# Kernel optimization log

Measured on AMD Instinct MI355X. Metric: run time of the kernel, lower is better.

The kernel has to match this reference:

```python
import jax, jax.numpy as jnp
import numpy as np

CONT_FIELD = 13
CATE_FIELD = 26
VOCAB = 100000
EMB_DIM = 64
HIDDEN = [1024, 1024]
B = 16384
N_FIELDS = CONT_FIELD + CATE_FIELD            # 39
COMB = N_FIELDS * (N_FIELDS - 1) // 2         # 741
FIRST = EMB_DIM * N_FIELDS + COMB             # 3237

# upper-triangular pair indices (i < j), matching the module's rows/cols
_ROWS, _COLS = np.triu_indices(N_FIELDS, k=1)
ROWS = jnp.asarray(_ROWS)
COLS = jnp.asarray(_COLS)


def setup_inputs() -> dict:
    key = jax.random.key(0)
    ks = jax.random.split(key, 12)
    a = np.square(3.0 / (CATE_FIELD * EMB_DIM))
    inp = {
        "conts": jax.random.uniform(ks[0], (B, CONT_FIELD), dtype=jnp.float32),
        "cates": jax.random.randint(ks[1], (B, CATE_FIELD), 0, VOCAB),
        "combs": jax.random.normal(ks[2], (B, COMB), dtype=jnp.float32),
        "emb_table": jax.random.uniform(ks[3], (VOCAB, EMB_DIM), minval=-a, maxval=a, dtype=jnp.float32),
        "W1": jax.random.normal(ks[4], (FIRST, HIDDEN[0]), dtype=jnp.float32) * (6.0 / (FIRST + HIDDEN[0])) ** 0.5,
        "b1": jnp.zeros((HIDDEN[0],), jnp.float32),
        "ln1_g": jnp.ones((HIDDEN[0],), jnp.float32),
        "ln1_b": jnp.zeros((HIDDEN[0],), jnp.float32),
        "W2": jax.random.normal(ks[5], (HIDDEN[0], HIDDEN[1]), dtype=jnp.float32) * (6.0 / (HIDDEN[0] + HIDDEN[1])) ** 0.5,
        "b2": jnp.zeros((HIDDEN[1],), jnp.float32),
        "ln2_g": jnp.ones((HIDDEN[1],), jnp.float32),
        "ln2_b": jnp.zeros((HIDDEN[1],), jnp.float32),
        "Wout": jax.random.normal(ks[6], (HIDDEN[1], 1), dtype=jnp.float32) * (6.0 / (HIDDEN[1] + 1)) ** 0.5,
        "bout": jnp.zeros((1,), jnp.float32),
    }
    return inp


def _layernorm(x, g, b, eps=1e-5):
    mu = jnp.mean(x, axis=-1, keepdims=True)
    var = jnp.mean((x - mu) ** 2, axis=-1, keepdims=True)
    return (x - mu) * jax.lax.rsqrt(var + eps) * g + b


def reference(conts, cates, combs, emb_table, W1, b1, ln1_g, ln1_b,
              W2, b2, ln2_g, ln2_b, Wout, bout):
    # continuous-field embeddings: rows 0..CONT_FIELD-1 of the table, scaled by values
    cont_emb = emb_table[:CONT_FIELD][None, :, :] * conts[:, :, None]   # [B, 13, D]
    cate_emb = emb_table[cates]                                          # [B, 26, D]
    cc = jnp.concatenate([cont_emb, cate_emb], axis=1)                   # [B, 39, D]
    # pairwise inner products: full Gram then upper-triangle extraction
    gram = jnp.einsum("bfd,bgd->bfg", cc, cc)                            # [B, 39, 39]
    pairs = gram[:, ROWS, COLS]                                          # [B, 741]
    X = jnp.concatenate([cont_emb.reshape(cc.shape[0], -1),
                         cate_emb.reshape(cc.shape[0], -1),
                         pairs], axis=1)                                  # [B, 3237]
    X = jax.nn.relu(_layernorm(X @ W1 + b1, ln1_g, ln1_b))
    X = jax.nn.relu(_layernorm(X @ W2 + b2, ln2_g, ln2_b))
    logit = jax.nn.sigmoid(X @ Wout + bout)                               # [B, 1]
    return logit
```

## Files before the change

### kernel.cpp

```cpp
#include <hip/hip_runtime.h>
#include <hip/hip_bf16.h>

#define BATCH 16384
#define NH 1024
#define NF 39
#define CCLD 72
#define KX 2432
#define NPAIR 741
#define FEAT_BLOCKS (BATCH / 4)
#define WPREP_BX (KX / 32 + NH / 32)
#define WPREP_BLOCKS (WPREP_BX * (NH / 32))

typedef __attribute__((ext_vector_type(8))) short bf16x8;
typedef __attribute__((ext_vector_type(4))) float f32x4;

typedef const __attribute__((address_space(1))) unsigned int* gptr_t;
typedef __attribute__((address_space(3))) unsigned int* lptr_t;

__device__ __forceinline__ float bf2f(unsigned short u) {
  union { unsigned int i; float f; } c; c.i = ((unsigned int)u) << 16; return c.f;
}
__device__ __forceinline__ unsigned short f2bf(float f) {
  union { float f; unsigned int i; } c; c.f = f;
  unsigned int r = c.i + 0x7FFFu + ((c.i >> 16) & 1u);
  return (unsigned short)(r >> 16);
}

__global__ __launch_bounds__(256) void prep_kernel(
    const float* __restrict__ conts, const int* __restrict__ cates,
    const float* __restrict__ emb, unsigned short* __restrict__ X,
    const float* __restrict__ W1, const float* __restrict__ W2,
    unsigned short* __restrict__ W1t, unsigned short* __restrict__ W2t) {
  __shared__ __align__(16) unsigned char smem[33664];

  if (blockIdx.x >= FEAT_BLOCKS) {
    int wq = blockIdx.x - FEAT_BLOCKS;
    int bx = wq % WPREP_BX;
    int nb = (wq / WPREP_BX) * 32;
    float (*tile)[33] = (float(*)[33])smem;
    int tx = threadIdx.x & 31, ty = threadIdx.x >> 5;
    if (bx < KX / 32) {
      int kb = bx * 32;
#pragma unroll
      for (int i = 0; i < 32; i += 8) {
        int k = kb + ty + i;
        float v = 0.f;
        if (k < 13) {
          float s = 0.f;
#pragma unroll 8
          for (int d = 0; d < 64; ++d)
            s += emb[k * 64 + d] * W1[(size_t)(k * 64 + d) * NH + nb + tx];
          v = s;
        } else if (k >= 16 && k < 1680) {
          v = W1[(size_t)(832 + k - 16) * NH + nb + tx];
        } else if (k >= 1680 && k < 1680 + NPAIR) {
          v = W1[(size_t)(2496 + k - 1680) * NH + nb + tx];
        }
        tile[ty + i][tx] = v;
      }
      __syncthreads();
#pragma unroll
      for (int i = 0; i < 32; i += 8)
        W1t[(size_t)(nb + ty + i) * KX + kb + tx] = f2bf(tile[tx][ty + i]);
    } else {
      int kb = (bx - KX / 32) * 32;
#pragma unroll
      for (int i = 0; i < 32; i += 8)
        tile[ty + i][tx] = W2[(size_t)(kb + ty + i) * NH + nb + tx];
      __syncthreads();
#pragma unroll
      for (int i = 0; i < 32; i += 8)
        W2t[(size_t)(nb + ty + i) * NH + kb + tx] = f2bf(tile[tx][ty + i]);
    }
    return;
  }

  int wid = threadIdx.x >> 6, lane = threadIdx.x & 63;
  int b = (blockIdx.x << 2) | wid;
  unsigned short* my = (unsigned short*)smem + wid * (48 * CCLD);
  unsigned short* pw = (unsigned short*)(smem + 27648) + wid * 752;
  unsigned short* Xrow = X + (size_t)b * KX;

  int2 c2[13];
#pragma unroll
  for (int i = 0; i < 13; ++i)
    c2[i] = ((const int2*)(cates + b * 26))[i];
  float cf[13];
#pragma unroll
  for (int f = 0; f < 13; ++f) cf[f] = conts[b * 13 + f];
  float cemb[13];
#pragma unroll
  for (int f = 0; f < 13; ++f) cemb[f] = emb[f * 64 + lane];
  float g[26];
#pragma unroll
  for (int j = 0; j < 26; ++j) {
    int idx = (j & 1) ? c2[j >> 1].y : c2[j >> 1].x;
    g[j] = emb[(size_t)idx * 64 + lane];
  }
#pragma unroll
  for (int f = 0; f < 13; ++f)
    my[f * CCLD + lane] = f2bf(cemb[f] * cf[f]);
#pragma unroll
  for (int j = 0; j < 26; ++j)
    my[(13 + j) * CCLD + lane] = f2bf(g[j]);
#pragma unroll
  for (int f = NF; f < 48; ++f) my[f * CCLD + lane] = 0;
  if (lane < 16) Xrow[lane] = (lane < 13) ? f2bf(cf[lane]) : 0;
  if (lane < 752 - NPAIR) pw[NPAIR + lane] = 0;
  __syncthreads();

#pragma unroll
  for (int i = 0; i < 4; ++i) {
    int q = i * 64 + lane;
    if (q < 208)
      *(bf16x8*)&Xrow[16 + q * 8] =
          *(const bf16x8*)&my[(13 + (q >> 3)) * CCLD + (q & 7) * 8];
  }

  int r15 = lane & 15, hi = lane >> 4;
  bf16x8 fr[2][3];
#pragma unroll
  for (int t = 0; t < 3; ++t)
#pragma unroll
    for (int h = 0; h < 2; ++h)
      fr[h][t] = *(const bf16x8*)&my[(t * 16 + r15) * CCLD + h * 32 + hi * 8];

  f32x4 acc[3][3];
#pragma unroll
  for (int it = 0; it < 3; ++it)
#pragma unroll
    for (int jt = 0; jt < 3; ++jt)
      acc[it][jt] = (f32x4){0.f, 0.f, 0.f, 0.f};
#pragma unroll
  for (int h = 0; h < 2; ++h)
#pragma unroll
    for (int it = 0; it < 3; ++it)
#pragma unroll
      for (int jt = 0; jt < 3; ++jt)
        acc[it][jt] = __builtin_amdgcn_mfma_f32_16x16x32_bf16(
            fr[h][it], fr[h][jt], acc[it][jt], 0, 0, 0);

#pragma unroll
  for (int it = 0; it < 3; ++it)
#pragma unroll
    for (int jt = 0; jt < 3; ++jt) {
      int g_ = jt * 16 + r15;
#pragma unroll
      for (int r = 0; r < 4; ++r) {
        int f = it * 16 + hi * 4 + r;
        if (f < g_ && g_ < NF) {
          int p = f * 38 - ((f * (f - 1)) >> 1) + g_ - f - 1;
          pw[p] = f2bf(acc[it][jt][r]);
        }
      }
    }
  __syncthreads();

#pragma unroll
  for (int i = 0; i < 2; ++i) {
    int q = i * 64 + lane;
    if (q < 94)
      *(bf16x8*)&Xrow[1680 + q * 8] = *(const bf16x8*)&pw[q * 8];
  }
}

#define GLL(s_, d_) __builtin_amdgcn_global_load_lds((gptr_t)(s_), (lptr_t)(d_), 16, 0, 0)
#define RD(p_) (*(const bf16x8*)(p_))
#define DSTA(buf, h) (lds + (buf) * 32768 + (h) * 8192 + sd)
#define DSTB(buf, h) (lds + (buf) * 32768 + 16384 + (h) * 8192 + sd)
#define STG(dst, srcb, tau) do { \
    const unsigned short* _s = (srcb) + (size_t)(tau) * 64; \
    GLL(_s, dst); GLL(_s + (size_t)64 * K, (dst) + 4096); } while (0)
#define PHASE_BAR() do { \
    __builtin_amdgcn_s_barrier(); \
    asm volatile("s_waitcnt lgkmcnt(0)" ::: "memory"); \
    __builtin_amdgcn_sched_barrier(0); \
    __builtin_amdgcn_s_setprio(1); } while (0)
#define PHASE_END() do { \
    __builtin_amdgcn_s_setprio(0); \
    __builtin_amdgcn_s_barrier(); \
    __builtin_amdgcn_sched_barrier(0); } while (0)
#define MQ(I0, J0, AB, BB) do { \
    _Pragma("unroll") \
    for (int i_ = 0; i_ < 4; ++i_) \
      _Pragma("unroll") \
      for (int j_ = 0; j_ < 2; ++j_) { \
        acc[(I0) + i_][(J0) + j_] = __builtin_amdgcn_mfma_f32_16x16x32_bf16( \
            AB[i_][0], BB[j_][0], acc[(I0) + i_][(J0) + j_], 0, 0, 0); \
        acc[(I0) + i_][(J0) + j_] = __builtin_amdgcn_mfma_f32_16x16x32_bf16( \
            AB[i_][1], BB[j_][1], acc[(I0) + i_][(J0) + j_], 0, 0, 0); \
      } } while (0)

__global__ __launch_bounds__(512, 2) void gemm_8ph(
    const unsigned short* __restrict__ A, const unsigned short* __restrict__ Bt,
    const float* __restrict__ bias, unsigned short* __restrict__ Hout,
    int K, int NT) {
  __shared__ unsigned short lds[65536];

  int bid = blockIdx.x;
  int swz = (bid & 7) * 32 + (bid >> 3);
  int mb = swz >> 2, nb = swz & 3;
  size_t m0 = (size_t)mb * 256, n0 = (size_t)nb * 256;

  int tid = threadIdx.x, lane = tid & 63, w = tid >> 6;
  int wr = w >> 2, wc = w & 3;
  int r15 = lane & 15, hi = lane >> 4;

  int sr = tid >> 3;
  int ce = ((tid & 7) ^ (sr & 7)) << 3;
  int sd = tid * 8;
  const unsigned short* A0p = A + (m0 + sr) * (size_t)K + ce;
  const unsigned short* A1p = A0p + (size_t)128 * K;
  const unsigned short* B0p = Bt + (n0 + sr) * (size_t)K + ce;
  const unsigned short* B1p = B0p + (size_t)128 * K;

  int cbs = (((hi << 4) ^ ((r15 & 7) << 4)) >> 1);
  int rb0 = r15 * 64 + cbs;
  int rb1 = rb0 ^ 32;
  const unsigned short* aH = lds + wr * 8192;
  const unsigned short* bH = lds + 16384 + (wc >> 1) * 8192 + (wc & 1) * 4096;

  f32x4 acc[8][4];
#pragma unroll
  for (int m = 0; m < 8; ++m)
#pragma unroll
    for (int n = 0; n < 4; ++n) acc[m][n] = (f32x4){0.f, 0.f, 0.f, 0.f};

  bf16x8 a0[4][2], a1[4][2], bS[2][2], bR[2][2];

  {
    int t1 = (NT > 1) ? 1 : 0;
    STG(DSTB(0, 0), B0p, 0);
    STG(DSTB(0, 1), B1p, 0);
    STG(DSTA(0, 0), A0p, 0);
    STG(DSTA(0, 1), A1p, 0);
    STG(DSTB(1, 0), B0p, t1);
    STG(DSTB(1, 1), B1p, t1);
    asm volatile("s_waitcnt vmcnt(4)" ::: "memory");
    __builtin_amdgcn_s_barrier();
    __builtin_amdgcn_sched_barrier(0);
#pragma unroll
    for (int i = 0; i < 4; ++i) {
      a0[i][0] = RD(aH + i * 1024 + rb0);
      a0[i][1] = RD(aH + i * 1024 + rb1);
    }
  }

  for (int t = 0; t < NT; ++t) {
    int cur = t & 1, nxt = cur ^ 1;
    int ta = (t + 1 < NT) ? t + 1 : NT - 1;
    int tb = (t + 2 < NT) ? t + 2 : NT - 1;
    const unsigned short* aBn = aH + nxt * 32768;
    const unsigned short* bB = bH + cur * 32768;

#pragma unroll
    for (int j = 0; j < 2; ++j) {
      bS[j][0] = RD(bB + j * 1024 + rb0);
      bS[j][1] = RD(bB + j * 1024 + rb1);
    }
    STG(DSTA(nxt, 0), A0p, ta);
    PHASE_BAR();
    MQ(0, 0, a0, bS);
    PHASE_END();

#pragma unroll
    for (int j = 0; j < 2; ++j) {
      bR[j][0] = RD(bB + (2 + j) * 1024 + rb0);
      bR[j][1] = RD(bB + (2 + j) * 1024 + rb1);
    }
#pragma unroll
    for (int i = 0; i < 4; ++i) {
      a1[i][0] = RD(aH + cur * 32768 + (4 + i) * 1024 + rb0);
      a1[i][1] = RD(aH + cur * 32768 + (4 + i) * 1024 + rb1);
    }
    STG(DSTA(nxt, 1), A1p, ta);
    __builtin_amdgcn_s_barrier();
    asm volatile("s_waitcnt lgkmcnt(8)" ::: "memory");
    __builtin_amdgcn_sched_barrier(0);
    __builtin_amdgcn_s_setprio(1);
    MQ(0, 2, a0, bR);
    PHASE_END();

    STG(DSTB(cur, 0), B0p, tb);
    PHASE_BAR();
    MQ(4, 2, a1, bR);
    PHASE_END();

    STG(DSTB(cur, 1), B1p, tb);
    asm volatile("s_waitcnt vmcnt(4)" ::: "memory");
    __builtin_amdgcn_s_barrier();
#pragma unroll
    for (int i = 0; i < 4; ++i) {
      a0[i][0] = RD(aBn + i * 1024 + rb0);
      a0[i][1] = RD(aBn + i * 1024 + rb1);
    }
    __builtin_amdgcn_sched_barrier(0);
    __builtin_amdgcn_s_setprio(1);
    MQ(4, 0, a1, bS);
    PHASE_END();
  }

  size_t crow = m0 + (size_t)wr * 128 + hi * 4;
  size_t ccol = n0 + (size_t)wc * 64 + r15;
  unsigned short* Hp = Hout + crow * NH + ccol;
  float bv[4];
#pragma unroll
  for (int n = 0; n < 4; ++n) bv[n] = bias[ccol + n * 16];
#pragma unroll
  for (int m = 0; m < 8; ++m)
#pragma unroll
    for (int n = 0; n < 4; ++n)
#pragma unroll
      for (int q = 0; q < 4; ++q)
        Hp[(size_t)(m * 16 + q) * NH + n * 16] = f2bf(acc[m][n][q] + bv[n]);
}

__global__ __launch_bounds__(256) void ln_relu_kernel(
    const unsigned short* __restrict__ Yb, const float* __restrict__ gamma,
    const float* __restrict__ beta, unsigned short* __restrict__ H) {
  int wid = threadIdx.x >> 6, lane = threadIdx.x & 63;
  int b = (blockIdx.x << 2) | wid;
  const unsigned short* yrow = Yb + (size_t)b * NH + lane * 16;
  bf16x8 u0 = *(const bf16x8*)&yrow[0];
  bf16x8 u1 = *(const bf16x8*)&yrow[8];
  float v[16];
#pragma unroll
  for (int i = 0; i < 8; ++i) {
    v[i] = bf2f((unsigned short)u0[i]);
    v[8 + i] = bf2f((unsigned short)u1[i]);
  }
  float s1 = 0.f, s2 = 0.f;
#pragma unroll
  for (int i = 0; i < 16; ++i) { s1 += v[i]; s2 += v[i] * v[i]; }
#pragma unroll
  for (int i = 1; i < 64; i <<= 1) {
    s1 += __shfl_xor(s1, i);
    s2 += __shfl_xor(s2, i);
  }
  float mu = s1 * (1.0f / NH);
  float var = s2 * (1.0f / NH) - mu * mu;
  float rs = rsqrtf(var + 1e-5f);
  const float4* gp = (const float4*)(gamma + lane * 16);
  const float4* bp = (const float4*)(beta + lane * 16);
  unsigned short o[16];
#pragma unroll
  for (int q = 0; q < 4; ++q) {
    float4 gg = gp[q], be = bp[q];
    o[q * 4 + 0] = f2bf(fmaxf((v[q * 4 + 0] - mu) * rs * gg.x + be.x, 0.f));
    o[q * 4 + 1] = f2bf(fmaxf((v[q * 4 + 1] - mu) * rs * gg.y + be.y, 0.f));
    o[q * 4 + 2] = f2bf(fmaxf((v[q * 4 + 2] - mu) * rs * gg.z + be.z, 0.f));
    o[q * 4 + 3] = f2bf(fmaxf((v[q * 4 + 3] - mu) * rs * gg.w + be.w, 0.f));
  }
  unsigned short* hrow = H + (size_t)b * NH + lane * 16;
  *(ulonglong2*)&hrow[0] = *(const ulonglong2*)&o[0];
  *(ulonglong2*)&hrow[8] = *(const ulonglong2*)&o[8];
}

__global__ __launch_bounds__(256) void ln_out_kernel(
    const unsigned short* __restrict__ Yb, const float* __restrict__ gamma,
    const float* __restrict__ beta, const float* __restrict__ Wout,
    const float* __restrict__ bout, float* __restrict__ out) {
  int wid = threadIdx.x >> 6, lane = threadIdx.x & 63;
  int b = (blockIdx.x << 2) | wid;
  const unsigned short* yrow = Yb + (size_t)b * NH + lane * 16;
  bf16x8 u0 = *(const bf16x8*)&yrow[0];
  bf16x8 u1 = *(const bf16x8*)&yrow[8];
  float v[16];
#pragma unroll
  for (int i = 0; i < 8; ++i) {
    v[i] = bf2f((unsigned short)u0[i]);
    v[8 + i] = bf2f((unsigned short)u1[i]);
  }
  float s1 = 0.f, s2 = 0.f;
#pragma unroll
  for (int i = 0; i < 16; ++i) { s1 += v[i]; s2 += v[i] * v[i]; }
#pragma unroll
  for (int i = 1; i < 64; i <<= 1) {
    s1 += __shfl_xor(s1, i);
    s2 += __shfl_xor(s2, i);
  }
  float mu = s1 * (1.0f / NH);
  float var = s2 * (1.0f / NH) - mu * mu;
  float rs = rsqrtf(var + 1e-5f);
  const float4* gp = (const float4*)(gamma + lane * 16);
  const float4* bp = (const float4*)(beta + lane * 16);
  const float4* wp = (const float4*)(Wout + lane * 16);
  float s = 0.f;
#pragma unroll
  for (int q = 0; q < 4; ++q) {
    float4 gg = gp[q], be = bp[q], wo = wp[q];
    s += fmaxf((v[q * 4 + 0] - mu) * rs * gg.x + be.x, 0.f) * wo.x;
    s += fmaxf((v[q * 4 + 1] - mu) * rs * gg.y + be.y, 0.f) * wo.y;
    s += fmaxf((v[q * 4 + 2] - mu) * rs * gg.z + be.z, 0.f) * wo.z;
    s += fmaxf((v[q * 4 + 3] - mu) * rs * gg.w + be.w, 0.f) * wo.w;
  }
#pragma unroll
  for (int i = 1; i < 64; i <<= 1) s += __shfl_xor(s, i);
  if (lane == 0) out[b] = 1.f / (1.f + expf(-(s + bout[0])));
}

extern "C" void kernel_launch(void* const* d_in, const int* in_sizes, int n_in,
                              void* d_out, int out_size, void* d_ws, size_t ws_size,
                              hipStream_t stream) {
  const float* conts = (const float*)d_in[0];
  const int* cates = (const int*)d_in[1];
  const float* emb  = (const float*)d_in[3];
  const float* W1   = (const float*)d_in[4];
  const float* b1   = (const float*)d_in[5];
  const float* ln1g = (const float*)d_in[6];
  const float* ln1b = (const float*)d_in[7];
  const float* W2   = (const float*)d_in[8];
  const float* b2   = (const float*)d_in[9];
  const float* ln2g = (const float*)d_in[10];
  const float* ln2b = (const float*)d_in[11];
  const float* Wout = (const float*)d_in[12];
  const float* bout = (const float*)d_in[13];
  float* out = (float*)d_out;

  unsigned short* X   = (unsigned short*)d_ws;
  unsigned short* W1t = X + (size_t)BATCH * KX;
  unsigned short* W2t = W1t + (size_t)NH * KX;
  unsigned short* H1  = W2t + (size_t)NH * NH;
  unsigned short* Yb1 = H1 + (size_t)BATCH * NH;
  unsigned short* Yb2 = Yb1 + (size_t)BATCH * NH;

  hipLaunchKernelGGL(prep_kernel, dim3(FEAT_BLOCKS + WPREP_BLOCKS), dim3(256), 0, stream,
                     conts, cates, emb, X, W1, W2, W1t, W2t);
  hipLaunchKernelGGL(gemm_8ph, dim3(256), dim3(512), 0, stream,
                     X, W1t, b1, Yb1, KX, KX / 64);
  hipLaunchKernelGGL(ln_relu_kernel, dim3(BATCH / 4), dim3(256), 0, stream,
                     Yb1, ln1g, ln1b, H1);
  hipLaunchKernelGGL(gemm_8ph, dim3(256), dim3(512), 0, stream,
                     H1, W2t, b2, Yb2, NH, NH / 64);
  hipLaunchKernelGGL(ln_out_kernel, dim3(BATCH / 4), dim3(256), 0, stream,
                     Yb2, ln2g, ln2b, Wout, bout, out);
}
```

Before: 171.1 us.

## Prefetch A two tiles ahead and cut per-iteration barriers in GEMM

Changes the GEMM main loop's staging so the A tiles, like the B tiles, are loaded two k-tiles ahead into the double buffer. All A and B stores for tile t+2 are issued after a single mid-iteration barrier. Most of the per-phase s_barrier pairs are removed, leaving two barriers per iteration plus waitcnt fences. This is meant to cut synchronisation overhead and give the global loads more time to hide behind MFMA work. The cost is more outstanding loads per wave, and getting buffer reuse wrong around the barriers could create LDS race hazards.

New measurement: 168.6 us. No clear change (-1.4%).

```diff
diff --git a/kernel.cpp b/kernel.cpp
--- a/kernel.cpp
+++ b/kernel.cpp
@@ -171,15 +171,7 @@
 #define STG(dst, srcb, tau) do { \
     const unsigned short* _s = (srcb) + (size_t)(tau) * 64; \
     GLL(_s, dst); GLL(_s + (size_t)64 * K, (dst) + 4096); } while (0)
-#define PHASE_BAR() do { \
-    __builtin_amdgcn_s_barrier(); \
-    asm volatile("s_waitcnt lgkmcnt(0)" ::: "memory"); \
-    __builtin_amdgcn_sched_barrier(0); \
-    __builtin_amdgcn_s_setprio(1); } while (0)
-#define PHASE_END() do { \
-    __builtin_amdgcn_s_setprio(0); \
-    __builtin_amdgcn_s_barrier(); \
-    __builtin_amdgcn_sched_barrier(0); } while (0)
+#define FENCE() __builtin_amdgcn_sched_barrier(0)
 #define MQ(I0, J0, AB, BB) do { \
     _Pragma("unroll") \
     for (int i_ = 0; i_ < 4; ++i_) \
@@ -230,15 +222,17 @@
 
   {
     int t1 = (NT > 1) ? 1 : 0;
+    STG(DSTA(0, 0), A0p, 0);
+    STG(DSTA(0, 1), A1p, 0);
     STG(DSTB(0, 0), B0p, 0);
     STG(DSTB(0, 1), B1p, 0);
-    STG(DSTA(0, 0), A0p, 0);
-    STG(DSTA(0, 1), A1p, 0);
+    STG(DSTA(1, 0), A0p, t1);
+    STG(DSTA(1, 1), A1p, t1);
     STG(DSTB(1, 0), B0p, t1);
     STG(DSTB(1, 1), B1p, t1);
-    asm volatile("s_waitcnt vmcnt(4)" ::: "memory");
-    __builtin_amdgcn_s_barrier();
-    __builtin_amdgcn_sched_barrier(0);
+    asm volatile("s_waitcnt vmcnt(8)" ::: "memory");
+    asm volatile("s_barrier" ::: "memory");
+    FENCE();
 #pragma unroll
     for (int i = 0; i < 4; ++i) {
       a0[i][0] = RD(aH + i * 1024 + rb0);
@@ -248,8 +242,8 @@
 
   for (int t = 0; t < NT; ++t) {
     int cur = t & 1, nxt = cur ^ 1;
-    int ta = (t + 1 < NT) ? t + 1 : NT - 1;
-    int tb = (t + 2 < NT) ? t + 2 : NT - 1;
+    int tc = (t + 2 < NT) ? t + 2 : NT - 1;
+    const unsigned short* aBc = aH + cur * 32768;
     const unsigned short* aBn = aH + nxt * 32768;
     const unsigned short* bB = bH + cur * 32768;
 
@@ -258,10 +252,12 @@
       bS[j][0] = RD(bB + j * 1024 + rb0);
       bS[j][1] = RD(bB + j * 1024 + rb1);
     }
-    STG(DSTA(nxt, 0), A0p, ta);
-    PHASE_BAR();
+    asm volatile("s_waitcnt lgkmcnt(0)" ::: "memory");
+    FENCE();
+    __builtin_amdgcn_s_setprio(1);
     MQ(0, 0, a0, bS);
-    PHASE_END();
+    __builtin_amdgcn_s_setprio(0);
+    FENCE();
 
 #pragma unroll
     for (int j = 0; j < 2; ++j) {
@@ -270,34 +266,40 @@
     }
 #pragma unroll
     for (int i = 0; i < 4; ++i) {
-      a1[i][0] = RD(aH + cur * 32768 + (4 + i) * 1024 + rb0);
-      a1[i][1] = RD(aH + cur * 32768 + (4 + i) * 1024 + rb1);
-    }
-    STG(DSTA(nxt, 1), A1p, ta);
-    __builtin_amdgcn_s_barrier();
+      a1[i][0] = RD(aBc + (4 + i) * 1024 + rb0);
+      a1[i][1] = RD(aBc + (4 + i) * 1024 + rb1);
+    }
     asm volatile("s_waitcnt lgkmcnt(8)" ::: "memory");
-    __builtin_amdgcn_sched_barrier(0);
+    FENCE();
     __builtin_amdgcn_s_setprio(1);
     MQ(0, 2, a0, bR);
-    PHASE_END();
-
-    STG(DSTB(cur, 0), B0p, tb);
-    PHASE_BAR();
+    __builtin_amdgcn_s_setprio(0);
+    asm volatile("s_waitcnt lgkmcnt(0)" ::: "memory");
+    asm volatile("s_barrier" ::: "memory");
+    FENCE();
+
+    STG(DSTB(cur, 0), B0p, tc);
+    STG(DSTA(cur, 0), A0p, tc);
+    STG(DSTA(cur, 1), A1p, tc);
+    __builtin_amdgcn_s_setprio(1);
     MQ(4, 2, a1, bR);
-    PHASE_END();
-
-    STG(DSTB(cur, 1), B1p, tb);
-    asm volatile("s_waitcnt vmcnt(4)" ::: "memory");
-    __builtin_amdgcn_s_barrier();
+    __builtin_amdgcn_s_setprio(0);
+    FENCE();
+
+    STG(DSTB(cur, 1), B1p, tc);
+    asm volatile("s_waitcnt vmcnt(8)" ::: "memory");
+    asm volatile("s_barrier" ::: "memory");
+    FENCE();
 #pragma unroll
     for (int i = 0; i < 4; ++i) {
       a0[i][0] = RD(aBn + i * 1024 + rb0);
       a0[i][1] = RD(aBn + i * 1024 + rb1);
     }
-    __builtin_amdgcn_sched_barrier(0);
+    FENCE();
     __builtin_amdgcn_s_setprio(1);
     MQ(4, 0, a1, bS);
-    PHASE_END();
+    __builtin_amdgcn_s_setprio(0);
+    FENCE();
   }
 
   size_t crow = m0 + (size_t)wr * 128 + hi * 4;
```
